# Kernel tuning notes

Hardware: AMD Instinct MI355X
Metric: run time of the kernel (lower is better)

The kernel has to match this reference:

```python
import jax, jax.numpy as jnp
import numpy as np

EPS = 1e-5  # torch BatchNorm default eps

def _bn(x, gamma, beta, axes):
    # training-mode batch norm: biased batch statistics over `axes`
    mean = jnp.mean(x, axis=axes, keepdims=True)
    var = jnp.var(x, axis=axes, keepdims=True)
    return gamma * (x - mean) / jnp.sqrt(var + EPS) + beta

def setup_inputs() -> dict:
    key = jax.random.key(0)
    ks = jax.random.split(key, 8)
    q, k, h, w, d, F = 64, 256, 8, 8, 512, 2048
    S = h * w  # seq_len = 64
    tgt = jax.random.normal(ks[0], (q, h, w, d), jnp.float32)
    memory = jax.random.normal(ks[1], (k, h, w, d), jnp.float32)
    W1 = jax.random.normal(ks[2], (d, d), jnp.float32) * 0.02
    b1 = jnp.zeros((d,), jnp.float32)
    se = jax.random.normal(ks[3], (S, S), jnp.float32)
    score_embed = (se + se.T).reshape(1, 1, S, S)  # symmetric, as in __init__
    W2 = jax.random.normal(ks[4], (F, S), jnp.float32) * 0.02
    b2 = jnp.zeros((F,), jnp.float32)
    W3 = jax.random.normal(ks[5], (1, F), jnp.float32) * 0.02
    b3 = jnp.zeros((1,), jnp.float32)
    g1 = jnp.ones((1,), jnp.float32); be1 = jnp.zeros((1,), jnp.float32)
    g2 = jnp.ones((F,), jnp.float32); be2 = jnp.zeros((F,), jnp.float32)
    g3 = jnp.ones((1,), jnp.float32); be3 = jnp.zeros((1,), jnp.float32)
    return dict(tgt=tgt, memory=memory, W1=W1, b1=b1, score_embed=score_embed,
                W2=W2, b2=b2, W3=W3, b3=b3,
                g1=g1, be1=be1, g2=g2, be2=be2, g3=g3, be3=be3, flag=1)

def reference(tgt, memory, W1, b1, score_embed, W2, b2, W3, b3,
              g1, be1, g2, be2, g3, be3, flag):
    q, h, w, d = tgt.shape
    kk = memory.shape[0]
    S = h * w
    tgt_f = tgt.reshape(q, S, d)
    mem_f = memory.reshape(kk, S, d)
    if flag:
        query = tgt_f @ W1.T + b1
        keym = mem_f @ W1.T + b1
        # [q, k, s, t] score tensor modulated by learned symmetric embedding
        score = jnp.einsum('qtd,ksd->qkst', query, keym) * jax.nn.sigmoid(score_embed)
    else:
        score = jnp.einsum('qtd,ksd->qkst', tgt_f, mem_f)
    score = score.reshape(q * kk, S, S)
    # dual-axis max pooling over score map, concatenated -> [q*k, 2S]
    score = jnp.concatenate([score.max(axis=1), score.max(axis=2)], axis=-1)
    x = score.reshape(-1, 1, S)                     # [2qk, 1, S]
    x = _bn(x, g1.reshape(1, 1, 1), be1.reshape(1, 1, 1), (0, 2)).reshape(-1, S)
    x = x @ W2.T + b2                               # [2qk, F]
    x = jax.nn.relu(_bn(x, g2, be2, (0,)))
    x = x @ W3.T + b3                               # [2qk, 1]
    x = x.reshape(-1, 2).sum(axis=-1, keepdims=True)  # [qk, 1]
    x = _bn(x, g3, be3, (0,))
    return x.reshape(q, kk)
```

## Files before the change

kernel.cpp:

```cpp
#include <hip/hip_runtime.h>
#include <hip/hip_bf16.h>
#include <math.h>
#include <float.h>

constexpr int NQ = 64, NK = 256, SSZ = 64, D = 512, FF = 2048;
constexpr int PAIRS = NQ * NK;
constexpr int ROWSX = 2 * PAIRS;
constexpr int NX = (NQ + NK) * SSZ;
constexpr int SBLK = 128;

typedef __bf16 bf16x8 __attribute__((ext_vector_type(8)));
typedef float floatx16 __attribute__((ext_vector_type(16)));

__device__ __forceinline__ void gl2lds16(const unsigned short* g, unsigned short* l) {
    __builtin_amdgcn_global_load_lds(
        (const __attribute__((address_space(1))) unsigned int*)(g),
        (__attribute__((address_space(3))) unsigned int*)(l),
        16, 0, 0);
}


__global__ __launch_bounds__(256) void k_cvt(
        const float* __restrict__ tgt, const float* __restrict__ mem,
        const float* __restrict__ W1, const float* __restrict__ W2,
        const float* __restrict__ se, const int* __restrict__ flag,
        __hip_bfloat16* __restrict__ Xb, __hip_bfloat16* __restrict__ W1b,
        __hip_bfloat16* __restrict__ W2b, float* __restrict__ sig) {
    constexpr int T4 = NQ * SSZ * D / 4;
    constexpr int X4 = NX * D / 4;
    constexpr int W4 = D * D / 4;
    constexpr int V4 = FF * 64 / 4;
    constexpr int S4 = SSZ * SSZ / 4;
    int idx = blockIdx.x * 256 + threadIdx.x;
    if (idx >= X4 + W4 + V4 + S4) return;
    if (idx >= X4 + W4 + V4) {
        int s = (idx - X4 - W4 - V4) * 4;
        float4 v = *reinterpret_cast<const float4*>(se + s);
        bool fl = (*flag) != 0;
        float4 o;
        o.x = fl ? 1.0f / (1.0f + expf(-v.x)) : 1.0f;
        o.y = fl ? 1.0f / (1.0f + expf(-v.y)) : 1.0f;
        o.z = fl ? 1.0f / (1.0f + expf(-v.z)) : 1.0f;
        o.w = fl ? 1.0f / (1.0f + expf(-v.w)) : 1.0f;
        *reinterpret_cast<float4*>(sig + s) = o;
        return;
    }
    const float* src;
    __hip_bfloat16* dst;
    if (idx < T4)           { src = tgt + (size_t)idx * 4;             dst = Xb + (size_t)idx * 4; }
    else if (idx < X4)      { src = mem + (size_t)(idx - T4) * 4;      dst = Xb + (size_t)idx * 4; }
    else if (idx < X4 + W4) { src = W1 + (size_t)(idx - X4) * 4;       dst = W1b + (size_t)(idx - X4) * 4; }
    else                    { src = W2 + (size_t)(idx - X4 - W4) * 4;  dst = W2b + (size_t)(idx - X4 - W4) * 4; }
    float4 v = *reinterpret_cast<const float4*>(src);
    union { __hip_bfloat16 h[4]; uint2 u; } o;
    o.h[0] = __float2bfloat16(v.x); o.h[1] = __float2bfloat16(v.y);
    o.h[2] = __float2bfloat16(v.z); o.h[3] = __float2bfloat16(v.w);
    *reinterpret_cast<uint2*>(dst) = o.u;
}

__global__ __launch_bounds__(256, 3) void k_gemm1_mfma(
        const __hip_bfloat16* __restrict__ Xb, const __hip_bfloat16* __restrict__ W1b,
        const float* __restrict__ b1, const int* __restrict__ flag,
        __hip_bfloat16* __restrict__ QKf) {
    __shared__ __attribute__((aligned(16))) unsigned short lds[2 * 128 * 64];
    const unsigned short* Xu = reinterpret_cast<const unsigned short*>(Xb);
    const unsigned short* Wu = reinterpret_cast<const unsigned short*>(W1b);
    unsigned short* Fu = reinterpret_cast<unsigned short*>(QKf);

    int tid = threadIdx.x;
    int bm = blockIdx.x >> 2, bn = blockIdx.x & 3;
    int m0 = bm * 128, n0 = bn * 128;

    if (!(*flag)) {
#pragma unroll
        for (int i = 0; i < 8; ++i) {
            int e = i * 256 + tid;
            int fb = e >> 6;
            int lp = e & 63;
            int rgl = fb >> 3, kgl = fb & 7;
            int row = m0 + rgl * 32 + (lp & 31);
            int col = n0 + kgl * 16 + (lp >> 5) * 8;
            uint4 v = *reinterpret_cast<const uint4*>(Xu + (size_t)row * D + col);
            size_t ofs = ((size_t)((m0 >> 5) + rgl) * 32 + (n0 >> 4) + kgl) * 512 + lp * 8;
            *reinterpret_cast<uint4*>(Fu + ofs) = v;
        }
        return;
    }

    int w = tid >> 6, l = tid & 63, h = l >> 5, c = l & 31;
    int wm = w >> 1, wn = w & 1;
    int chg = (l & 7) ^ (l >> 3);
    int cx = c & 7;
    floatx16 acc00 = {}, acc01 = {}, acc10 = {}, acc11 = {};

    for (int kb = 0; kb < D; kb += 64) {
#pragma unroll
        for (int j = 0; j < 8; ++j) {
            int i = w * 8 + j;
            int buf = i >> 4;
            int rb = (i & 15) * 8;
            int r = rb + (l >> 3);
            const unsigned short* src = (buf == 0)
                ? (Xu + (size_t)(m0 + r) * D + kb + chg * 8)
                : (Wu + (size_t)(n0 + r) * D + kb + chg * 8);
            gl2lds16(src, lds + buf * 8192 + rb * 64);
        }
        __syncthreads();
        const unsigned short* pA = lds + (wm * 64) * 64;
        const unsigned short* pB = lds + 8192 + (wn * 64) * 64;
#pragma unroll
        for (int st = 0; st < 4; ++st) {
            int ko = ((st * 2 + h) ^ cx) * 8;
            bf16x8 a0 = *reinterpret_cast<const bf16x8*>(pA + c * 64 + ko);
            bf16x8 a1 = *reinterpret_cast<const bf16x8*>(pA + (32 + c) * 64 + ko);
            bf16x8 b0 = *reinterpret_cast<const bf16x8*>(pB + c * 64 + ko);
            bf16x8 b1v = *reinterpret_cast<const bf16x8*>(pB + (32 + c) * 64 + ko);
            acc00 = __builtin_amdgcn_mfma_f32_32x32x16_bf16(b0, a0, acc00, 0, 0, 0);
            acc01 = __builtin_amdgcn_mfma_f32_32x32x16_bf16(b0, a1, acc01, 0, 0, 0);
            acc10 = __builtin_amdgcn_mfma_f32_32x32x16_bf16(b1v, a0, acc10, 0, 0, 0);
            acc11 = __builtin_amdgcn_mfma_f32_32x32x16_bf16(b1v, a1, acc11, 0, 0, 0);
        }
        __syncthreads();
    }

#pragma unroll
    for (int ni = 0; ni < 2; ++ni) {
        int nb = n0 + wn * 64 + ni * 32;
#pragma unroll
        for (int mi = 0; mi < 2; ++mi) {
            const floatx16& A = ni ? (mi ? acc11 : acc10) : (mi ? acc01 : acc00);
            int mb = m0 + wm * 64 + mi * 32;
            size_t rgbase = ((size_t)(mb >> 5) * 32 + (nb >> 4)) * 512;
#pragma unroll
            for (int g = 0; g < 4; ++g) {
                float4 bia = *reinterpret_cast<const float4*>(&b1[nb + 8 * g + 4 * h]);
                union { __hip_bfloat16 hh[4]; uint2 u; } o;
                o.hh[0] = __float2bfloat16(A[4 * g + 0] + bia.x);
                o.hh[1] = __float2bfloat16(A[4 * g + 1] + bia.y);
                o.hh[2] = __float2bfloat16(A[4 * g + 2] + bia.z);
                o.hh[3] = __float2bfloat16(A[4 * g + 3] + bia.w);
                *reinterpret_cast<uint2*>(Fu + rgbase + (size_t)(g >> 1) * 512
                                          + (c + 32 * (g & 1)) * 8 + 4 * h) = o.u;
            }
        }
    }
}

__global__ __launch_bounds__(512, 2) void k_score_mfma(
        const __hip_bfloat16* __restrict__ QKf, const float* __restrict__ sig,
        float* __restrict__ xbuf) {
    __shared__ __attribute__((aligned(16))) unsigned short lds[65536];
    const unsigned short* Fu = reinterpret_cast<const unsigned short*>(QKf);

    int tid = threadIdx.x;
    int w = tid >> 6, l = tid & 63, h = l >> 5, c = l & 31;
    int qig = blockIdx.x >> 5, ktg = blockIdx.x & 31;
    int kt = ktg * 8 + w;

    const unsigned short* Qg = Fu + (size_t)qig * 65536;
#pragma unroll
    for (int i = 0; i < 16; ++i) {
        int e = i * 512 + tid;
        gl2lds16(Qg + e * 8, lds + e * 8);
    }

    const unsigned short* pK0 = Fu + (size_t)(128 + kt * 2) * 16384 + l * 8;
    const unsigned short* pK1 = pK0 + 16384;

    floatx16 acc[2][4] = {};
    bf16x8 ka0[2][4], ka1[2][4];
#pragma unroll
    for (int st = 0; st < 4; ++st) {
        ka0[0][st] = *reinterpret_cast<const bf16x8*>(pK0 + st * 512);
        ka1[0][st] = *reinterpret_cast<const bf16x8*>(pK1 + st * 512);
    }
    __syncthreads();

    const unsigned short* qlds = lds + l * 8;
#pragma unroll
    for (int kbi = 0; kbi < 8; ++kbi) {
        const int cur = kbi & 1, nxt = cur ^ 1;
        if (kbi < 7) {
            pK0 += 2048; pK1 += 2048;
#pragma unroll
            for (int st = 0; st < 4; ++st) {
                ka0[nxt][st] = *reinterpret_cast<const bf16x8*>(pK0 + st * 512);
                ka1[nxt][st] = *reinterpret_cast<const bf16x8*>(pK1 + st * 512);
            }
        }
#pragma unroll
        for (int g = 0; g < 4; ++g) {
            bf16x8 qb[4];
#pragma unroll
            for (int st = 0; st < 4; ++st)
                qb[st] = *reinterpret_cast<const bf16x8*>(qlds + (g * 32 + kbi * 4 + st) * 512);
            __builtin_amdgcn_s_setprio(1);
#pragma unroll
            for (int st = 0; st < 4; ++st) {
                acc[0][g] = __builtin_amdgcn_mfma_f32_32x32x16_bf16(ka0[cur][st], qb[st], acc[0][g], 0, 0, 0);
                acc[1][g] = __builtin_amdgcn_mfma_f32_32x32x16_bf16(ka1[cur][st], qb[st], acc[1][g], 0, 0, 0);
            }
            __builtin_amdgcn_s_setprio(0);
        }
    }

    const float* sigl = sig;

    int p0 = (qig * 2) * 256 + kt;
    int p1 = p0 + 256;
    float tmax[4] = {-FLT_MAX, -FLT_MAX, -FLT_MAX, -FLT_MAX};
#pragma unroll
    for (int sh = 0; sh < 2; ++sh) {
        float smA[16], smB[16];
#pragma unroll
        for (int r = 0; r < 16; ++r) {
            int srow = sh * 32 + (r & 3) + 8 * (r >> 2) + 4 * h;
            float s0 = sigl[srow * 64 + c];
            float s1 = sigl[srow * 64 + 32 + c];
            float v0 = acc[sh][0][r] * s0;
            float v1 = acc[sh][1][r] * s1;
            float v2 = acc[sh][2][r] * s0;
            float v3 = acc[sh][3][r] * s1;
            tmax[0] = fmaxf(tmax[0], v0);
            tmax[1] = fmaxf(tmax[1], v1);
            tmax[2] = fmaxf(tmax[2], v2);
            tmax[3] = fmaxf(tmax[3], v3);
            smA[r] = fmaxf(v0, v1);
            smB[r] = fmaxf(v2, v3);
        }
#pragma unroll
        for (int stage = 1; stage < 32; stage <<= 1)
#pragma unroll
            for (int r = 0; r < 16; ++r) {
                smA[r] = fmaxf(smA[r], __shfl_xor(smA[r], stage, 64));
                smB[r] = fmaxf(smB[r], __shfl_xor(smB[r], stage, 64));
            }
        if (c == 0) {
#pragma unroll
            for (int r = 0; r < 16; ++r) {
                int srow = sh * 32 + (r & 3) + 8 * (r >> 2) + 4 * h;
                xbuf[(size_t)(2 * p0 + 1) * 64 + srow] = smA[r];
                xbuf[(size_t)(2 * p1 + 1) * 64 + srow] = smB[r];
            }
        }
    }
#pragma unroll
    for (int g = 0; g < 4; ++g)
        tmax[g] = fmaxf(tmax[g], __shfl_xor(tmax[g], 32, 64));
    if (h == 0) {
        xbuf[(size_t)(2 * p0) * 64 + c] = tmax[0];
        xbuf[(size_t)(2 * p0) * 64 + 32 + c] = tmax[1];
        xbuf[(size_t)(2 * p1) * 64 + c] = tmax[2];
        xbuf[(size_t)(2 * p1) * 64 + 32 + c] = tmax[3];
    }
}

__global__ __launch_bounds__(256) void k_stats1(const float* __restrict__ xbuf,
        float* __restrict__ S1p, float* __restrict__ S2p) {
    __shared__ float xr[8][64];
    int tid = threadIdx.x;
    int row0 = blockIdx.x * 256;
    float acc[16] = {};
    float s1 = 0.f;
    int a = tid >> 2;
    int bbase = (tid & 3) * 16;
    int lr = tid >> 5, lc = (tid & 31) * 2;
    for (int it = 0; it < 32; ++it) {
        int r = row0 + it * 8;
        *reinterpret_cast<float2*>(&xr[lr][lc]) =
            *reinterpret_cast<const float2*>(&xbuf[(size_t)(r + lr) * 64 + lc]);
        __syncthreads();
        float xa[8];
#pragma unroll
        for (int j = 0; j < 8; ++j) xa[j] = xr[j][a];
#pragma unroll
        for (int j = 0; j < 8; ++j) {
            const float4* pb = reinterpret_cast<const float4*>(&xr[j][bbase]);
            float4 b0 = pb[0], b1 = pb[1], b2 = pb[2], b3 = pb[3];
            acc[0] += xa[j] * b0.x;  acc[1] += xa[j] * b0.y;
            acc[2] += xa[j] * b0.z;  acc[3] += xa[j] * b0.w;
            acc[4] += xa[j] * b1.x;  acc[5] += xa[j] * b1.y;
            acc[6] += xa[j] * b1.z;  acc[7] += xa[j] * b1.w;
            acc[8] += xa[j] * b2.x;  acc[9] += xa[j] * b2.y;
            acc[10] += xa[j] * b2.z; acc[11] += xa[j] * b2.w;
            acc[12] += xa[j] * b3.x; acc[13] += xa[j] * b3.y;
            acc[14] += xa[j] * b3.z; acc[15] += xa[j] * b3.w;
        }
        if (tid < 64) {
#pragma unroll
            for (int j = 0; j < 8; ++j) s1 += xr[j][tid];
        }
        __syncthreads();
    }
    float* dst = S2p + (size_t)blockIdx.x * 4096 + tid * 16;
#pragma unroll
    for (int e = 0; e < 16; e += 4)
        *reinterpret_cast<float4*>(dst + e) = make_float4(acc[e], acc[e+1], acc[e+2], acc[e+3]);
    if (tid < 64) S1p[blockIdx.x * 64 + tid] = s1;
}

__global__ __launch_bounds__(256) void k_red(const float* __restrict__ S1p,
        const float* __restrict__ S2p, float* __restrict__ S1f,
        float* __restrict__ S2f) {
    __shared__ double part[4][64];
    int tid = threadIdx.x;
    int il = tid & 63, bq = tid >> 6;
    int idx = blockIdx.x * 64 + il;
    double s = 0.0;
    for (int b = bq * 32; b < bq * 32 + 32; ++b)
        s += (double)S2p[(size_t)b * 4096 + idx];
    part[bq][il] = s;
    __syncthreads();
    if (tid < 64) {
        double t = part[0][tid] + part[1][tid] + part[2][tid] + part[3][tid];
        S2f[blockIdx.x * 64 + tid] = (float)t;
    }
    if (blockIdx.x == 0 && tid >= 64 && tid < 128) {
        int j = tid - 64;
        double s1 = 0.0;
        for (int b = 0; b < SBLK; ++b) s1 += (double)S1p[b * 64 + j];
        S1f[j] = (float)s1;
    }
}

__global__ __launch_bounds__(256) void k_bn2(
        const float* __restrict__ S1f, const float* __restrict__ S2f,
        const __hip_bfloat16* __restrict__ W2b,
        const float* __restrict__ g1, const float* __restrict__ be1,
        const float* __restrict__ g2, const float* __restrict__ be2,
        float* __restrict__ alpha, float* __restrict__ beta) {
    __shared__ float mb[64];
    __shared__ float scal[3];
    int tid = threadIdx.x;
    const float Rinvf = 1.0f / (float)ROWSX;
    if (tid < 64) {
        double ss = (double)S1f[tid];
        double sq = (double)S2f[tid * 65];
#pragma unroll
        for (int off = 32; off; off >>= 1) {
            ss += __shfl_down(ss, off);
            sq += __shfl_down(sq, off);
        }
        if (tid == 0) {
            const double Nall = (double)ROWSX * 64.0;
            double m1 = ss / Nall;
            double var1 = sq / Nall - m1 * m1;
            double scaled = (double)g1[0] / sqrt(var1 + 1e-5);
            scal[0] = (float)(scaled * scaled);
            scal[1] = (float)m1;
            scal[2] = (float)scaled;
        }
        mb[tid] = S1f[tid] * Rinvf;
    }
    __syncthreads();
    int w = tid >> 6;
    int j = tid & 63;
    int f = blockIdx.x * 4 + w;
    float wj = __bfloat162float(W2b[(size_t)f * 64 + j]);
    float mj = mb[j];
    float t1 = 0.f;
    for (int b = 0; b < 64; ++b)
        t1 += (S2f[j * 64 + b] * Rinvf - mj * mb[b]) * __bfloat162float(W2b[(size_t)f * 64 + b]);
    float vc = wj * t1 * scal[0];
    float xbj = (mj - scal[1]) * scal[2] + be1[0];
    float mc = wj * xbj;
#pragma unroll
    for (int off = 32; off; off >>= 1) {
        vc += __shfl_down(vc, off);
        mc += __shfl_down(mc, off);
    }
    if (j == 0) {
        float t2 = g2[f] * rsqrtf(vc + 1e-5f);
        alpha[f] = t2;
        beta[f] = -t2 * mc + be2[f];
    }
}

__global__ __launch_bounds__(256, 4) void k_mlp_mfma(
        const float* __restrict__ xbuf, const float* __restrict__ S1f,
        const float* __restrict__ S2f, const float* __restrict__ g1,
        const float* __restrict__ be1, const __hip_bfloat16* __restrict__ W2b,
        const float* __restrict__ alpha, const float* __restrict__ beta,
        const float* __restrict__ W3, const float* __restrict__ b3,
        float* __restrict__ z) {
    constexpr int LDR = 72;
    __shared__ __attribute__((aligned(16))) unsigned short Xs[128 * LDR];
    __shared__ __attribute__((aligned(16))) unsigned short Ws[128 * LDR];
    __shared__ float abw[3 * 128];
    __shared__ float scl[2];
    const unsigned short* W2u = reinterpret_cast<const unsigned short*>(W2b);
    int tid = threadIdx.x;
    int w = tid >> 6, l = tid & 63, h = l >> 5, c = l & 31;
    int r0 = blockIdx.x * 128;

    if (tid < 64) {
        double ss = (double)S1f[tid];
        double sq = (double)S2f[tid * 65];
#pragma unroll
        for (int off = 32; off; off >>= 1) {
            ss += __shfl_down(ss, off);
            sq += __shfl_down(sq, off);
        }
        if (tid == 0) {
            const double Nall = (double)ROWSX * 64.0;
            double m1 = ss / Nall;
            double var1 = sq / Nall - m1 * m1;
            scl[0] = (float)m1;
            scl[1] = (float)((double)g1[0] / sqrt(var1 + 1e-5));
        }
    }
    __syncthreads();
    float m1 = scl[0], sc = scl[1], sh = be1[0];

#pragma unroll
    for (int i = 0; i < 4; ++i) {
        int id = i * 256 + tid;
        int row = id >> 3, cg = id & 7;
        const float* src = xbuf + (size_t)(r0 + row) * 64 + cg * 8;
        float4 v0 = *reinterpret_cast<const float4*>(src);
        float4 v1 = *reinterpret_cast<const float4*>(src + 4);
        union { __hip_bfloat16 hh[8]; uint4 u; } o;
        o.hh[0] = __float2bfloat16((v0.x - m1) * sc + sh);
        o.hh[1] = __float2bfloat16((v0.y - m1) * sc + sh);
        o.hh[2] = __float2bfloat16((v0.z - m1) * sc + sh);
        o.hh[3] = __float2bfloat16((v0.w - m1) * sc + sh);
        o.hh[4] = __float2bfloat16((v1.x - m1) * sc + sh);
        o.hh[5] = __float2bfloat16((v1.y - m1) * sc + sh);
        o.hh[6] = __float2bfloat16((v1.z - m1) * sc + sh);
        o.hh[7] = __float2bfloat16((v1.w - m1) * sc + sh);
        *reinterpret_cast<uint4*>(&Xs[row * LDR + cg * 8]) = o.u;
    }

    float zacc[16] = {};
    for (int fc = 0; fc < FF / 128; ++fc) {
#pragma unroll
        for (int i = 0; i < 4; ++i) {
            int id = i * 256 + tid;
            int row = id >> 3, cg = id & 7;
            uint4 v = *reinterpret_cast<const uint4*>(W2u + (size_t)(fc * 128 + row) * 64 + cg * 8);
            *reinterpret_cast<uint4*>(&Ws[row * LDR + cg * 8]) = v;
        }
        if (tid < 128) {
            int f = fc * 128 + tid;
            abw[tid] = alpha[f];
            abw[128 + tid] = beta[f];
            abw[256 + tid] = W3[f];
        }
        __syncthreads();
        bf16x8 a[4];
#pragma unroll
        for (int st = 0; st < 4; ++st)
            a[st] = *reinterpret_cast<const bf16x8*>(&Xs[(w * 32 + c) * LDR + st * 16 + h * 8]);
#pragma unroll
        for (int nq = 0; nq < 4; ++nq) {
            floatx16 u = {};
#pragma unroll
            for (int st = 0; st < 4; ++st) {
                bf16x8 b = *reinterpret_cast<const bf16x8*>(&Ws[(nq * 32 + c) * LDR + st * 16 + h * 8]);
                u = __builtin_amdgcn_mfma_f32_32x32x16_bf16(a[st], b, u, 0, 0, 0);
            }
            float al = abw[nq * 32 + c];
            float bt = abw[128 + nq * 32 + c];
            float w3 = abw[256 + nq * 32 + c];
#pragma unroll
            for (int r = 0; r < 16; ++r)
                zacc[r] += fmaxf(al * u[r] + bt, 0.f) * w3;
        }
        __syncthreads();
    }
#pragma unroll
    for (int stage = 1; stage < 32; stage <<= 1)
#pragma unroll
        for (int r = 0; r < 16; ++r)
            zacc[r] += __shfl_xor(zacc[r], stage, 64);
    if (c == 0) {
        float bb = b3[0];
#pragma unroll
        for (int r = 0; r < 16; ++r) {
            int row = r0 + w * 32 + (r & 3) + 8 * (r >> 2) + 4 * h;
            z[row] = zacc[r] + bb;
        }
    }
}

__global__ __launch_bounds__(256) void k_pair(const float* __restrict__ z,
        float* __restrict__ v, double* __restrict__ sums3) {
    int i = blockIdx.x * 256 + threadIdx.x;
    float val = z[2 * i] + z[2 * i + 1];
    v[i] = val;
    float s = val, ss = val * val;
#pragma unroll
    for (int off = 32; off; off >>= 1) {
        s += __shfl_down(s, off);
        ss += __shfl_down(ss, off);
    }
    __shared__ float bs[4], bss[4];
    int lane = threadIdx.x & 63, w = threadIdx.x >> 6;
    if (lane == 0) { bs[w] = s; bss[w] = ss; }
    __syncthreads();
    if (threadIdx.x == 0) {
        atomicAdd(&sums3[0], (double)(bs[0] + bs[1] + bs[2] + bs[3]));
        atomicAdd(&sums3[1], (double)(bss[0] + bss[1] + bss[2] + bss[3]));
    }
}

__global__ __launch_bounds__(256) void k_out(const float* __restrict__ v,
        const double* __restrict__ sums3, const float* __restrict__ g3,
        const float* __restrict__ be3, float* __restrict__ out) {
    double m = sums3[0] / (double)PAIRS;
    double var = sums3[1] / (double)PAIRS - m * m;
    float mm = (float)m;
    float inv = (float)((double)g3[0] / sqrt(var + 1e-5));
    int i = blockIdx.x * 256 + threadIdx.x;
    if (i < PAIRS) out[i] = (v[i] - mm) * inv + be3[0];
}

extern "C" void kernel_launch(void* const* d_in, const int* in_sizes, int n_in,
                              void* d_out, int out_size, void* d_ws, size_t ws_size,
                              hipStream_t stream) {
    (void)in_sizes; (void)n_in; (void)out_size; (void)ws_size;
    const float* tgt = (const float*)d_in[0];
    const float* mem = (const float*)d_in[1];
    const float* W1  = (const float*)d_in[2];
    const float* b1  = (const float*)d_in[3];
    const float* se  = (const float*)d_in[4];
    const float* W2  = (const float*)d_in[5];
    const float* b2  = (const float*)d_in[6];
    const float* W3  = (const float*)d_in[7];
    const float* b3  = (const float*)d_in[8];
    const float* g1  = (const float*)d_in[9];
    const float* be1 = (const float*)d_in[10];
    const float* g2  = (const float*)d_in[11];
    const float* be2 = (const float*)d_in[12];
    const float* g3  = (const float*)d_in[13];
    const float* be3 = (const float*)d_in[14];
    const int*  flag = (const int*)d_in[15];
    (void)b2;
    float* out = (float*)d_out;

    char* ws = (char*)d_ws;
    size_t off = 0;
    auto alloc = [&](size_t bytes) -> void* {
        void* p = ws + off;
        off = (off + bytes + 255) & ~(size_t)255;
        return p;
    };
    float* sig   = (float*)alloc((size_t)SSZ * SSZ * 4);
    __hip_bfloat16* Xb  = (__hip_bfloat16*)alloc((size_t)NX * D * 2);
    __hip_bfloat16* W1b = (__hip_bfloat16*)alloc((size_t)D * D * 2);
    __hip_bfloat16* W2b = (__hip_bfloat16*)alloc((size_t)FF * 64 * 2);
    __hip_bfloat16* QKf = (__hip_bfloat16*)alloc((size_t)NX * D * 2);
    float* xbuf  = (float*)alloc((size_t)ROWSX * 64 * 4);
    float* z     = (float*)alloc((size_t)ROWSX * 4);
    float* v     = (float*)alloc((size_t)PAIRS * 4);
    float* alpha = (float*)alloc((size_t)FF * 4);
    float* beta  = (float*)alloc((size_t)FF * 4);
    float* S1p   = (float*)alloc((size_t)SBLK * 64 * 4);
    float* S2p   = (float*)alloc((size_t)SBLK * 4096 * 4);
    float* S1f   = (float*)alloc(64 * 4);
    float* S2f   = (float*)alloc(4096 * 4);
    size_t statsStart = off;
    double* sums3 = (double*)alloc(2 * 8);
    size_t statsEnd = off;

    hipMemsetAsync(ws + statsStart, 0, statsEnd - statsStart, stream);

    constexpr int CVT4 = (NX * D + D * D + FF * 64) / 4;
    constexpr int SIG4 = SSZ * SSZ / 4;
    k_cvt<<<(CVT4 + SIG4 + 255) / 256, 256, 0, stream>>>(
        tgt, mem, W1, W2, se, flag, Xb, W1b, W2b, sig);
    k_gemm1_mfma<<<(NX / 128) * (D / 128), 256, 0, stream>>>(Xb, W1b, b1, flag, QKf);
    k_score_mfma<<<(NQ / 2) * (NK / 8), 512, 0, stream>>>(QKf, sig, xbuf);
    k_stats1<<<SBLK, 256, 0, stream>>>(xbuf, S1p, S2p);
    k_red<<<64, 256, 0, stream>>>(S1p, S2p, S1f, S2f);
    k_bn2<<<FF / 4, 256, 0, stream>>>(S1f, S2f, W2b, g1, be1, g2, be2, alpha, beta);
    k_mlp_mfma<<<ROWSX / 128, 256, 0, stream>>>(xbuf, S1f, S2f, g1, be1, W2b,
                                                alpha, beta, W3, b3, z);
    k_pair<<<PAIRS / 256, 256, 0, stream>>>(z, v, sums3);
    k_out<<<PAIRS / 256, 256, 0, stream>>>(v, sums3, g3, be3, out);
}
```

Before: 293.0 us.

## Split MLP kernel over F chunks, double stats blocks, cache S2 in LDS

The MLP kernel is now split four ways along the hidden dimension F. Each block handles a quarter of the F tiles and writes partial z values into a 4x buffer, which k_pair then sums. This quadruples grid size to improve occupancy, at the cost of recomputing the per-block setup and extra global traffic. Separately, k_stats1 uses twice as many blocks over fewer rows each, and k_bn2 caches the S2 matrix in padded shared memory instead of reading it strided from global memory.

Result: no change. 290.5 us (-0.8%).

```diff
diff --git a/kernel.cpp b/kernel.cpp
--- a/kernel.cpp
+++ b/kernel.cpp
@@ -7,7 +7,7 @@
 constexpr int PAIRS = NQ * NK;
 constexpr int ROWSX = 2 * PAIRS;
 constexpr int NX = (NQ + NK) * SSZ;
-constexpr int SBLK = 128;
+constexpr int SBLK = 256;
 
 typedef __bf16 bf16x8 __attribute__((ext_vector_type(8)));
 typedef float floatx16 __attribute__((ext_vector_type(16)));
@@ -259,13 +259,13 @@
         float* __restrict__ S1p, float* __restrict__ S2p) {
     __shared__ float xr[8][64];
     int tid = threadIdx.x;
-    int row0 = blockIdx.x * 256;
+    int row0 = blockIdx.x * 128;
     float acc[16] = {};
     float s1 = 0.f;
     int a = tid >> 2;
     int bbase = (tid & 3) * 16;
     int lr = tid >> 5, lc = (tid & 31) * 2;
-    for (int it = 0; it < 32; ++it) {
+    for (int it = 0; it < 16; ++it) {
         int r = row0 + it * 8;
         *reinterpret_cast<float2*>(&xr[lr][lc]) =
             *reinterpret_cast<const float2*>(&xbuf[(size_t)(r + lr) * 64 + lc]);
@@ -307,7 +307,7 @@
     int il = tid & 63, bq = tid >> 6;
     int idx = blockIdx.x * 64 + il;
     double s = 0.0;
-    for (int b = bq * 32; b < bq * 32 + 32; ++b)
+    for (int b = bq * 64; b < bq * 64 + 64; ++b)
         s += (double)S2p[(size_t)b * 4096 + idx];
     part[bq][il] = s;
     __syncthreads();
@@ -329,10 +329,16 @@
         const float* __restrict__ g1, const float* __restrict__ be1,
         const float* __restrict__ g2, const float* __restrict__ be2,
         float* __restrict__ alpha, float* __restrict__ beta) {
+    __shared__ float S2c[64 * 65];
     __shared__ float mb[64];
     __shared__ float scal[3];
     int tid = threadIdx.x;
     const float Rinvf = 1.0f / (float)ROWSX;
+#pragma unroll
+    for (int i = 0; i < 16; ++i) {
+        int idx = i * 256 + tid;
+        S2c[(idx >> 6) * 65 + (idx & 63)] = S2f[idx];
+    }
     if (tid < 64) {
         double ss = (double)S1f[tid];
         double sq = (double)S2f[tid * 65];
@@ -360,7 +366,7 @@
     float mj = mb[j];
     float t1 = 0.f;
     for (int b = 0; b < 64; ++b)
-        t1 += (S2f[j * 64 + b] * Rinvf - mj * mb[b]) * __bfloat162float(W2b[(size_t)f * 64 + b]);
+        t1 += (S2c[j * 65 + b] * Rinvf - mj * mb[b]) * __bfloat162float(W2b[(size_t)f * 64 + b]);
     float vc = wj * t1 * scal[0];
     float xbj = (mj - scal[1]) * scal[2] + be1[0];
     float mc = wj * xbj;
@@ -382,7 +388,7 @@
         const float* __restrict__ be1, const __hip_bfloat16* __restrict__ W2b,
         const float* __restrict__ alpha, const float* __restrict__ beta,
         const float* __restrict__ W3, const float* __restrict__ b3,
-        float* __restrict__ z) {
+        float* __restrict__ z4) {
     constexpr int LDR = 72;
     __shared__ __attribute__((aligned(16))) unsigned short Xs[128 * LDR];
     __shared__ __attribute__((aligned(16))) unsigned short Ws[128 * LDR];
@@ -391,7 +397,8 @@
     const unsigned short* W2u = reinterpret_cast<const unsigned short*>(W2b);
     int tid = threadIdx.x;
     int w = tid >> 6, l = tid & 63, h = l >> 5, c = l & 31;
-    int r0 = blockIdx.x * 128;
+    int rb = blockIdx.x >> 2, q = blockIdx.x & 3;
+    int r0 = rb * 128;
 
     if (tid < 64) {
         double ss = (double)S1f[tid];
@@ -432,7 +439,8 @@
     }
 
     float zacc[16] = {};
-    for (int fc = 0; fc < FF / 128; ++fc) {
+    for (int fci = 0; fci < 4; ++fci) {
+        int fc = q * 4 + fci;
 #pragma unroll
         for (int i = 0; i < 4; ++i) {
             int id = i * 256 + tid;
@@ -474,19 +482,22 @@
         for (int r = 0; r < 16; ++r)
             zacc[r] += __shfl_xor(zacc[r], stage, 64);
     if (c == 0) {
-        float bb = b3[0];
+        float bb = (q == 0) ? b3[0] : 0.f;
 #pragma unroll
         for (int r = 0; r < 16; ++r) {
             int row = r0 + w * 32 + (r & 3) + 8 * (r >> 2) + 4 * h;
-            z[row] = zacc[r] + bb;
-        }
-    }
-}
-
-__global__ __launch_bounds__(256) void k_pair(const float* __restrict__ z,
+            z4[(size_t)q * ROWSX + row] = zacc[r] + bb;
+        }
+    }
+}
+
+__global__ __launch_bounds__(256) void k_pair(const float* __restrict__ z4,
         float* __restrict__ v, double* __restrict__ sums3) {
     int i = blockIdx.x * 256 + threadIdx.x;
-    float val = z[2 * i] + z[2 * i + 1];
+    float val = 0.f;
+#pragma unroll
+    for (int q = 0; q < 4; ++q)
+        val += z4[(size_t)q * ROWSX + 2 * i] + z4[(size_t)q * ROWSX + 2 * i + 1];
     v[i] = val;
     float s = val, ss = val * val;
 #pragma unroll
@@ -551,7 +562,7 @@
     __hip_bfloat16* W2b = (__hip_bfloat16*)alloc((size_t)FF * 64 * 2);
     __hip_bfloat16* QKf = (__hip_bfloat16*)alloc((size_t)NX * D * 2);
     float* xbuf  = (float*)alloc((size_t)ROWSX * 64 * 4);
-    float* z     = (float*)alloc((size_t)ROWSX * 4);
+    float* z4    = (float*)alloc((size_t)4 * ROWSX * 4);
     float* v     = (float*)alloc((size_t)PAIRS * 4);
     float* alpha = (float*)alloc((size_t)FF * 4);
     float* beta  = (float*)alloc((size_t)FF * 4);
@@ -574,8 +585,8 @@
     k_stats1<<<SBLK, 256, 0, stream>>>(xbuf, S1p, S2p);
     k_red<<<64, 256, 0, stream>>>(S1p, S2p, S1f, S2f);
     k_bn2<<<FF / 4, 256, 0, stream>>>(S1f, S2f, W2b, g1, be1, g2, be2, alpha, beta);
-    k_mlp_mfma<<<ROWSX / 128, 256, 0, stream>>>(xbuf, S1f, S2f, g1, be1, W2b,
-                                                alpha, beta, W3, b3, z);
-    k_pair<<<PAIRS / 256, 256, 0, stream>>>(z, v, sums3);
+    k_mlp_mfma<<<(ROWSX / 128) * 4, 256, 0, stream>>>(xbuf, S1f, S2f, g1, be1, W2b,
+                                                      alpha, beta, W3, b3, z4);
+    k_pair<<<PAIRS / 256, 256, 0, stream>>>(z4, v, sums3);
     k_out<<<PAIRS / 256, 256, 0, stream>>>(v, sums3, g3, be3, out);
 }
```
